# Kernel optimization log

Measured on AMD Instinct MI355X. Metric: run time of the kernel, lower is better.

Reference implementation:

```python
import jax, jax.numpy as jnp
import numpy as np

EMBED_DIM = 1024
HEAD_NUM = 16
HEAD_DIM = EMBED_DIM // HEAD_NUM
T, B, S = 2048, 4, 2048


def setup_inputs() -> dict:
    key = jax.random.key(0)
    ks = jax.random.split(key, 11)
    s = 0.02
    return {
        "query": jax.random.normal(ks[0], (T, B, EMBED_DIM), jnp.float32),
        "key": jax.random.normal(ks[1], (S, B, EMBED_DIM), jnp.float32),
        "value": jax.random.normal(ks[2], (S, B, EMBED_DIM), jnp.float32),
        "q_proj_weight": jax.random.normal(ks[3], (EMBED_DIM, EMBED_DIM), jnp.float32) * s,
        "k_proj_weight": jax.random.normal(ks[4], (EMBED_DIM, EMBED_DIM), jnp.float32) * s,
        "v_proj_weight": jax.random.normal(ks[5], (EMBED_DIM, EMBED_DIM), jnp.float32) * s,
        "in_proj_bias": jax.random.normal(ks[6], (3 * EMBED_DIM,), jnp.float32) * s,
        "bias_k": jax.random.normal(ks[7], (1, 1, EMBED_DIM), jnp.float32) * s,
        "bias_v": jax.random.normal(ks[8], (1, 1, EMBED_DIM), jnp.float32) * s,
        "out_proj_weight": jax.random.normal(ks[9], (EMBED_DIM, EMBED_DIM), jnp.float32) * s,
        "out_proj_bias": jax.random.normal(ks[10], (EMBED_DIM,), jnp.float32) * s,
    }


def reference(query, key, value, q_proj_weight, k_proj_weight, v_proj_weight,
              in_proj_bias, bias_k, bias_v, out_proj_weight, out_proj_bias):
    t, b, e = query.shape
    h, hd = HEAD_NUM, HEAD_DIM
    scaling = float(hd) ** -0.5
    # input projections (F.linear: x @ W.T + b)
    q = (query @ q_proj_weight.T + in_proj_bias[:e]) * scaling          # [T,B,E]
    k = key @ k_proj_weight.T + in_proj_bias[e:2 * e]                   # [S,B,E]
    v = value @ v_proj_weight.T + in_proj_bias[2 * e:]                  # [S,B,E]
    # append bias_k / bias_v token along the sequence dim
    k = jnp.concatenate([k, jnp.broadcast_to(bias_k, (1, b, e))], axis=0)  # [S+1,B,E]
    v = jnp.concatenate([v, jnp.broadcast_to(bias_v, (1, b, e))], axis=0)  # [S+1,B,E]
    # split heads: [L, B, E] -> [B*H, L, hd]
    q = q.reshape(t, b * h, hd).transpose(1, 0, 2)
    k = k.reshape(-1, b * h, hd).transpose(1, 0, 2)
    v = v.reshape(-1, b * h, hd).transpose(1, 0, 2)
    # full O(T*S) attention, as in the original bmm->softmax->bmm
    weights = jax.nn.softmax(jnp.einsum('nqd,nkd->nqk', q, k), axis=-1)  # [B*H,T,S+1]
    out = jnp.einsum('nqk,nkd->nqd', weights, v)                         # [B*H,T,hd]
    out = out.transpose(1, 0, 2).reshape(t, b, e)
    out = out @ out_proj_weight.T + out_proj_bias
    avg_weights = weights.sum(axis=1) / h                                # [B*H,S+1]
    return out, avg_weights
```

## Files before the change

kernel.cpp:

```cpp
#include <hip/hip_runtime.h>

#define T_DIM 2048
#define B_DIM 4
#define S_DIM 2048
#define E_DIM 1024
#define H_NUM 16
#define HD    64
#define NH    64
#define SP1   2049
#define SPAD  2112
#define NCHUNK 33
#define NTOKE ((size_t)T_DIM * B_DIM * E_DIM)

typedef short bf16x8 __attribute__((ext_vector_type(8)));
typedef short bf16x4 __attribute__((ext_vector_type(4)));
typedef float f32x4  __attribute__((ext_vector_type(4)));
typedef float f32x16 __attribute__((ext_vector_type(16)));
typedef unsigned int u32;

#define QSCALE 0.18033688011112042f

#if __has_builtin(__builtin_amdgcn_exp2f)
__device__ __forceinline__ float exp2_fast(float x) { return __builtin_amdgcn_exp2f(x); }
#else
__device__ __forceinline__ float exp2_fast(float x) { return __expf(x * 0.6931471805599453f); }
#endif

__device__ __forceinline__ unsigned short f2bf(float x) {
    union { float f; unsigned int u; } v; v.f = x;
    unsigned int r = v.u + 0x7FFFu + ((v.u >> 16) & 1u);
    return (unsigned short)(r >> 16);
}

__device__ __forceinline__ u32 cvtpk_bf16(float lo, float hi) {
    u32 r;
    asm("v_cvt_pk_bf16_f32 %0, %1, %2" : "=v"(r) : "v"(lo), "v"(hi));
    return r;
}
__device__ __forceinline__ void plswap(u32& a, u32& b) {
    asm("v_permlane32_swap_b32 %0, %1" : "+v"(a), "+v"(b));
}
__device__ __forceinline__ float max3f(float a, float b, float c) {
    float d;
    asm("v_max3_f32 %0, %1, %2, %3" : "=v"(d) : "v"(a), "v"(b), "v"(c));
    return d;
}

__device__ __forceinline__ void load_lds16(const void* g, void* l) {
    __builtin_amdgcn_global_load_lds(
        (const __attribute__((address_space(1))) unsigned int*)g,
        (__attribute__((address_space(3))) unsigned int*)l, 16, 0, 0);
}

__global__ __launch_bounds__(256)
void cvt_all(const float* __restrict__ q, const float* __restrict__ k,
             const float* __restrict__ v, const float* __restrict__ w0,
             const float* __restrict__ w1, const float* __restrict__ w2,
             const float* __restrict__ w3, short* __restrict__ indst,
             short* __restrict__ wdst, short* __restrict__ k_h,
             short* __restrict__ v_h, const float* __restrict__ bias_k,
             const float* __restrict__ bias_v)
{
    const int y = blockIdx.y;
    if (y < 3) {
        const float* src = (y == 0) ? q : (y == 1) ? k : v;
        short* d = indst + (size_t)y * NTOKE;
        const size_t i = (size_t)blockIdx.x * 256 + threadIdx.x;
        const float4* s = reinterpret_cast<const float4*>(src) + i * 2;
        float4 a = s[0], b = s[1];
        uint4 o;
        o.x = cvtpk_bf16(a.x, a.y); o.y = cvtpk_bf16(a.z, a.w);
        o.z = cvtpk_bf16(b.x, b.y); o.w = cvtpk_bf16(b.z, b.w);
        *(reinterpret_cast<uint4*>(d) + i) = o;
    } else {
        const size_t gi = (size_t)blockIdx.x * 256 + threadIdx.x;
        const size_t per = (size_t)E_DIM * E_DIM / 8;
        if (gi < 4 * per) {
            const int wsel = (int)(gi / per);
            const size_t i = gi % per;
            const float* src = (wsel == 0) ? w0 : (wsel == 1) ? w1 : (wsel == 2) ? w2 : w3;
            short* d = wdst + (size_t)wsel * E_DIM * E_DIM;
            const float4* s = reinterpret_cast<const float4*>(src) + i * 2;
            float4 a = s[0], b = s[1];
            uint4 o;
            o.x = cvtpk_bf16(a.x, a.y); o.y = cvtpk_bf16(a.z, a.w);
            o.z = cvtpk_bf16(b.x, b.y); o.w = cvtpk_bf16(b.z, b.w);
            *(reinterpret_cast<uint4*>(d) + i) = o;
        } else {
            const size_t fi = gi - 4 * per;
            if (fi < (size_t)(SPAD - S_DIM) * NH * HD) {
                const int d   = (int)(fi & 63);
                const int row = (int)((fi >> 6) & 63);
                const int n   = (int)(fi >> 12);
                short bk = 0, bv = 0;
                if (row == 0) {
                    bk = (short)f2bf(bias_k[(n & 15) * HD + d]);
                    bv = (short)f2bf(bias_v[(n & 15) * HD + d]);
                }
                const size_t idx = ((size_t)n * SPAD + S_DIM + row) * HD + d;
                k_h[idx] = bk;
                v_h[idx] = bv;
            }
        }
    }
}

__global__ __launch_bounds__(256, 4)
void gemm_qkv(const short* __restrict__ Abase, const short* __restrict__ Wall,
              const float* __restrict__ biasAll, short* __restrict__ outp)
{
    __shared__ short smem[16384];
    short* Asb = smem;
    short* Bsb = smem + 8192;

    const int id = blockIdx.x;
    const int xcd = id & 7;
    const int j = id >> 3;
    const int z = j >> 6;
    const int jj = j & 63;
    const int bm = xcd * 8 + (jj & 7);
    const int bn = jj >> 3;

    const short* Az = Abase + (size_t)z * NTOKE;
    const short* W  = Wall + (size_t)z * E_DIM * E_DIM;
    const float* bias = biasAll + z * E_DIM;

    const int tid = threadIdx.x;
    const int l = tid & 63, w = tid >> 6;
    const int wr = w >> 1, wc = w & 1;
    const int lr = l & 15, lg = l >> 4;
    const int srow = tid >> 2, scol = (tid & 3) * 8;

    auto stage = [&](int b, int k0) {
#pragma unroll
        for (int r = 0; r < 2; ++r) {
            const int row = r * 64 + srow;
            load_lds16(Az + (size_t)(bm * 128 + row) * E_DIM + k0 + scol,
                       Asb + b * 4096 + row * 32 + scol);
            load_lds16(W + (size_t)(bn * 128 + row) * E_DIM + k0 + scol,
                       Bsb + b * 4096 + row * 32 + scol);
        }
    };

    stage(0, 0);
    stage(1, 32);

    f32x4 acc[4][4] = {};
    int buf = 0;

    for (int k0 = 0; k0 < E_DIM; k0 += 32) {
        if (k0 + 32 < E_DIM)
            asm volatile("s_waitcnt vmcnt(4)" ::: "memory");
        else
            asm volatile("s_waitcnt vmcnt(0)" ::: "memory");
        asm volatile("s_barrier" ::: "memory");
        __builtin_amdgcn_sched_barrier(0);

        __builtin_amdgcn_s_setprio(1);
        bf16x8 af[4], bf[4];
#pragma unroll
        for (int mi = 0; mi < 4; ++mi)
            af[mi] = *reinterpret_cast<const bf16x8*>(
                Asb + buf * 4096 + (wr * 64 + mi * 16 + lr) * 32 + lg * 8);
#pragma unroll
        for (int ni = 0; ni < 4; ++ni)
            bf[ni] = *reinterpret_cast<const bf16x8*>(
                Bsb + buf * 4096 + (wc * 64 + ni * 16 + lr) * 32 + lg * 8);
#pragma unroll
        for (int mi = 0; mi < 4; ++mi)
#pragma unroll
            for (int ni = 0; ni < 4; ++ni)
                acc[mi][ni] = __builtin_amdgcn_mfma_f32_16x16x32_bf16(
                    af[mi], bf[ni], acc[mi][ni], 0, 0, 0);
        __builtin_amdgcn_s_setprio(0);

        asm volatile("s_barrier" ::: "memory");
        if (k0 + 64 < E_DIM) stage(buf, k0 + 64);
        buf ^= 1;
    }

#pragma unroll
    for (int mi = 0; mi < 4; ++mi)
#pragma unroll
        for (int ni = 0; ni < 4; ++ni) {
            const int colg = bn * 128 + wc * 64 + ni * 16 + lr;
            const float bv = bias[colg];
            const int cl = wc * 64 + ni * 16 + lr;
#pragma unroll
            for (int r = 0; r < 4; ++r) {
                float v = acc[mi][ni][r] + bv;
                if (z == 0) v *= QSCALE;
                const int rowl = wr * 64 + mi * 16 + lg * 4 + r;
                smem[rowl * 128 + cl] = (short)f2bf(v);
            }
        }
    __syncthreads();

    short* ob = outp;
    if (z == 1) ob += (size_t)NH * T_DIM * HD;
    else if (z == 2) ob += (size_t)NH * T_DIM * HD + (size_t)NH * SPAD * HD;
    const int sd = (z == 0) ? T_DIM : SPAD;
#pragma unroll
    for (int p = 0; p < 8; ++p) {
        const int Ls = p * 2048 + tid * 8;
        const int rowl = Ls >> 7;
        const int col  = Ls & 127;
        const int m = bm * 128 + rowl;
        const int seq = m >> 2, b = m & 3;
        const int colg = bn * 128 + col;
        const int head = colg >> 6, d = colg & 63;
        *reinterpret_cast<uint4*>(ob + ((size_t)(b * 16 + head) * sd + seq) * HD + d) =
            *reinterpret_cast<const uint4*>(smem + Ls);
    }
}

__global__ __launch_bounds__(256, 2)
void gemm_out(const short* __restrict__ o_h, const short* __restrict__ wob,
              const float* __restrict__ out_b, float* __restrict__ out)
{
    __shared__ short As[2][128][64];
    __shared__ short Bs[2][128][64];

    const int id = blockIdx.x;
    const int xcd = id & 7;
    const int j = id >> 3;
    const int bm = xcd * 8 + (j & 7);
    const int bn = j >> 3;

    const int tid = threadIdx.x;
    const int l = tid & 63, w = tid >> 6;
    const int wr = w >> 1, wc = w & 1;
    const int lr = l & 15, lg = l >> 4;
    const int srow = tid >> 3, scol = (tid & 7) * 8;

    auto stage = [&](int b, int k0) {
#pragma unroll
        for (int r = 0; r < 4; ++r) {
            const int row = r * 32 + srow;
            const int m = bm * 128 + row;
            const short* ga = o_h +
                ((size_t)((m & 3) * 16 + (k0 >> 6)) * T_DIM + (m >> 2)) * HD + scol;
            load_lds16(ga, &As[b][row][scol]);
            load_lds16(wob + (size_t)(bn * 128 + row) * E_DIM + k0 + scol, &Bs[b][row][scol]);
        }
    };

    stage(0, 0);
    __syncthreads();

    f32x4 acc[4][4] = {};
    int buf = 0;

    for (int k0 = 0; k0 < E_DIM; k0 += 64) {
        if (k0 + 64 < E_DIM) stage(buf ^ 1, k0 + 64);

        __builtin_amdgcn_s_setprio(1);
#pragma unroll
        for (int c = 0; c < 2; ++c) {
            bf16x8 af[4], bf[4];
#pragma unroll
            for (int mi = 0; mi < 4; ++mi)
                af[mi] = *reinterpret_cast<const bf16x8*>(&As[buf][wr * 64 + mi * 16 + lr][c * 32 + lg * 8]);
#pragma unroll
            for (int ni = 0; ni < 4; ++ni)
                bf[ni] = *reinterpret_cast<const bf16x8*>(&Bs[buf][wc * 64 + ni * 16 + lr][c * 32 + lg * 8]);
#pragma unroll
            for (int mi = 0; mi < 4; ++mi)
#pragma unroll
                for (int ni = 0; ni < 4; ++ni)
                    acc[mi][ni] = __builtin_amdgcn_mfma_f32_16x16x32_bf16(
                        af[mi], bf[ni], acc[mi][ni], 0, 0, 0);
        }
        __builtin_amdgcn_s_setprio(0);
        __syncthreads();
        buf ^= 1;
    }

#pragma unroll
    for (int mi = 0; mi < 4; ++mi)
#pragma unroll
        for (int ni = 0; ni < 4; ++ni) {
            const int colg = bn * 128 + wc * 64 + ni * 16 + lr;
            const float bv = out_b[colg];
#pragma unroll
            for (int r = 0; r < 4; ++r) {
                const int m = bm * 128 + wr * 64 + mi * 16 + lg * 4 + r;
                out[(size_t)m * E_DIM + colg] = acc[mi][ni][r] + bv;
            }
        }
}

__global__ __launch_bounds__(512, 4)
void attn_mfma(const short* __restrict__ q_h, const short* __restrict__ k_h,
               const short* __restrict__ v_h, short* __restrict__ o_h,
               float* __restrict__ m_arr, float* __restrict__ l_arr)
{
    __shared__ short KsD[2][64 * 64];
    __shared__ short VtD[2][64 * 64];

    const int id = blockIdx.x;
    const int xcd = id & 7, slot = id >> 3;
    const int n = xcd * 8 + (slot >> 3);
    const int q0 = (slot & 7) * 256;

    const int tid = threadIdx.x, l = tid & 63, w = tid >> 6;
    const int ql = l & 31;
    const int hi = l >> 5;
    const int qrow = q0 + w * 32 + ql;

    const int krow = tid >> 3, kcg = tid & 7;
    const int kswz = (kcg * 16) ^ ((krow & 7) << 4);
    const int sp = tid & 31, dq = tid >> 5;

    const short* kbase = k_h + (size_t)n * SPAD * HD;
    const short* vbase = v_h + (size_t)n * SPAD * HD;

    bf16x8 aq0, aq1, aq2, aq3;
    {
        const short* qp = q_h + ((size_t)n * T_DIM + qrow) * HD + hi * 8;
        aq0 = *(const bf16x8*)(qp);
        aq1 = *(const bf16x8*)(qp + 16);
        aq2 = *(const bf16x8*)(qp + 32);
        aq3 = *(const bf16x8*)(qp + 48);
    }

    bf16x8 pk  = *(const bf16x8*)(kbase + (size_t)krow * HD + kcg * 8);
    bf16x4 pva = *(const bf16x4*)(vbase + (size_t)(2 * sp) * HD + dq * 4);
    bf16x4 pvb = *(const bf16x4*)(vbase + (size_t)(2 * sp + 1) * HD + dq * 4);
    {
        char* KsB = (char*)KsD[0];
        char* VtB = (char*)VtD[0];
        *(bf16x8*)(KsB + krow * 128 + kswz) = pk;
#pragma unroll
        for (int j = 0; j < 4; ++j) {
            u32 pkd = (u32)(unsigned short)pva[j] | ((u32)(unsigned short)pvb[j] << 16);
            const int d = dq * 4 + j;
            *(u32*)(VtB + d * 128 + ((4 * sp) ^ ((d & 7) << 4))) = pkd;
        }
    }
    __syncthreads();

    float m_run = 0.0f;
    float l_run = 0.0f;
    f32x16 accA, accB;
#pragma unroll
    for (int r = 0; r < 16; ++r) { accA[r] = 0.f; accB[r] = 0.f; }

    for (int kc = 0; kc < NCHUNK; ++kc) {
        const char* KsB = (const char*)KsD[kc & 1];
        const char* VtB = (const char*)VtD[kc & 1];
        const bool more = (kc + 1 < NCHUNK);

        if (more) {
            const int s0n = (kc + 1) * 64;
            pk  = *(const bf16x8*)(kbase + (size_t)(s0n + krow) * HD + kcg * 8);
            pva = *(const bf16x4*)(vbase + (size_t)(s0n + 2 * sp) * HD + dq * 4);
            pvb = *(const bf16x4*)(vbase + (size_t)(s0n + 2 * sp + 1) * HD + dq * 4);
        }

        f32x16 sc0, sc1;
        const float nm = -m_run;
#pragma unroll
        for (int r = 0; r < 16; ++r) { sc0[r] = nm; sc1[r] = nm; }
        __builtin_amdgcn_s_setprio(1);
#pragma unroll
        for (int sl = 0; sl < 4; ++sl) {
            const int cb = ((sl * 32) + hi * 16) ^ ((ql & 7) << 4);
            bf16x8 kf0 = *(const bf16x8*)(KsB + ql * 128 + cb);
            bf16x8 kf1 = *(const bf16x8*)(KsB + (32 + ql) * 128 + cb);
            bf16x8 qf = (sl == 0) ? aq0 : (sl == 1) ? aq1 : (sl == 2) ? aq2 : aq3;
            sc0 = __builtin_amdgcn_mfma_f32_32x32x16_bf16(kf0, qf, sc0, 0, 0, 0);
            sc1 = __builtin_amdgcn_mfma_f32_32x32x16_bf16(kf1, qf, sc1, 0, 0, 0);
        }
        __builtin_amdgcn_s_setprio(0);

        const int s0 = kc * 64;
        if (s0 + 64 > SP1) {
#pragma unroll
            for (int r = 0; r < 16; ++r) {
                const int key = (r & 3) + 8 * (r >> 2) + 4 * hi;
                if (s0 + key >= SP1)      sc0[r] = -1e30f;
                if (s0 + 32 + key >= SP1) sc1[r] = -1e30f;
            }
        }

        float a0 = max3f(sc0[0],  sc0[1],  sc0[2]);
        float a1 = max3f(sc0[3],  sc0[4],  sc0[5]);
        float a2 = max3f(sc0[6],  sc0[7],  sc0[8]);
        float a3 = max3f(sc0[9],  sc0[10], sc0[11]);
        float a4 = max3f(sc0[12], sc0[13], sc0[14]);
        float a5 = max3f(sc0[15], sc1[0],  sc1[1]);
        float a6 = max3f(sc1[2],  sc1[3],  sc1[4]);
        float a7 = max3f(sc1[5],  sc1[6],  sc1[7]);
        float a8 = max3f(sc1[8],  sc1[9],  sc1[10]);
        float a9 = max3f(sc1[11], sc1[12], sc1[13]);
        float aA = fmaxf(sc1[14], sc1[15]);
        float b0 = max3f(a0, a1, a2);
        float b1 = max3f(a3, a4, a5);
        float b2 = max3f(a6, a7, a8);
        float b3 = fmaxf(a9, aA);
        float mxl = fmaxf(max3f(b0, b1, b2), b3);
        const float mx = fmaxf(mxl, __shfl_xor(mxl, 32));
        if (!__all(mx <= 8.0f)) {
            const float sh = fmaxf(mx, 0.0f);
            const float fac = exp2_fast(-sh);
            l_run *= fac;
#pragma unroll
            for (int r = 0; r < 16; ++r) {
                accA[r] *= fac; accB[r] *= fac;
                sc0[r] -= sh;   sc1[r] -= sh;
            }
            m_run += sh;
        }
        float p0[16], p1[16];
#pragma unroll
        for (int r = 0; r < 16; ++r) p0[r] = exp2_fast(sc0[r]);
#pragma unroll
        for (int r = 0; r < 16; ++r) p1[r] = exp2_fast(sc1[r]);
        float sv[16];
#pragma unroll
        for (int r = 0; r < 16; ++r) sv[r] = p0[r] + p1[r];
#pragma unroll
        for (int s = 8; s > 0; s >>= 1)
#pragma unroll
            for (int r = 0; r < s; ++r) sv[r] += sv[r + s];
        l_run += sv[0] + __shfl_xor(sv[0], 32);

        union PF { u32 u[4]; bf16x8 v; };
        PF pf0, pf1, pf2, pf3;
        {
            u32 a0_ = cvtpk_bf16(p0[0], p0[1]),   b0_ = cvtpk_bf16(p0[4], p0[5]);   plswap(a0_, b0_);
            u32 a1_ = cvtpk_bf16(p0[2], p0[3]),   b1_ = cvtpk_bf16(p0[6], p0[7]);   plswap(a1_, b1_);
            u32 a2_ = cvtpk_bf16(p0[8], p0[9]),   b2_ = cvtpk_bf16(p0[12], p0[13]); plswap(a2_, b2_);
            u32 a3_ = cvtpk_bf16(p0[10], p0[11]), b3_ = cvtpk_bf16(p0[14], p0[15]); plswap(a3_, b3_);
            pf0.u[0] = a0_; pf0.u[1] = a1_; pf0.u[2] = b0_; pf0.u[3] = b1_;
            pf1.u[0] = a2_; pf1.u[1] = a3_; pf1.u[2] = b2_; pf1.u[3] = b3_;
            u32 c0_ = cvtpk_bf16(p1[0], p1[1]),   d0_ = cvtpk_bf16(p1[4], p1[5]);   plswap(c0_, d0_);
            u32 c1_ = cvtpk_bf16(p1[2], p1[3]),   d1_ = cvtpk_bf16(p1[6], p1[7]);   plswap(c1_, d1_);
            u32 c2_ = cvtpk_bf16(p1[8], p1[9]),   d2_ = cvtpk_bf16(p1[12], p1[13]); plswap(c2_, d2_);
            u32 c3_ = cvtpk_bf16(p1[10], p1[11]), d3_ = cvtpk_bf16(p1[14], p1[15]); plswap(c3_, d3_);
            pf2.u[0] = c0_; pf2.u[1] = c1_; pf2.u[2] = d0_; pf2.u[3] = d1_;
            pf3.u[0] = c2_; pf3.u[1] = c3_; pf3.u[2] = d2_; pf3.u[3] = d3_;
        }

        __builtin_amdgcn_s_setprio(1);
#pragma unroll
        for (int ksl = 0; ksl < 4; ++ksl) {
            const int cb = ((ksl * 32) + hi * 16) ^ ((ql & 7) << 4);
            bf16x8 vf0 = *(const bf16x8*)(VtB + ql * 128 + cb);
            bf16x8 vf1 = *(const bf16x8*)(VtB + (32 + ql) * 128 + cb);
            const bf16x8 pv = (ksl == 0) ? pf0.v : (ksl == 1) ? pf1.v : (ksl == 2) ? pf2.v : pf3.v;
            accA = __builtin_amdgcn_mfma_f32_32x32x16_bf16(vf0, pv, accA, 0, 0, 0);
            accB = __builtin_amdgcn_mfma_f32_32x32x16_bf16(vf1, pv, accB, 0, 0, 0);
        }
        __builtin_amdgcn_s_setprio(0);

        if (more) {
            char* KsN = (char*)KsD[(kc & 1) ^ 1];
            char* VtN = (char*)VtD[(kc & 1) ^ 1];
            *(bf16x8*)(KsN + krow * 128 + kswz) = pk;
#pragma unroll
            for (int j = 0; j < 4; ++j) {
                u32 pkd = (u32)(unsigned short)pva[j] | ((u32)(unsigned short)pvb[j] << 16);
                const int d = dq * 4 + j;
                *(u32*)(VtN + d * 128 + ((4 * sp) ^ ((d & 7) << 4))) = pkd;
            }
            __syncthreads();
        }
    }

    const float il = 1.0f / l_run;
    short* orow = o_h + ((size_t)n * T_DIM + qrow) * HD;
#pragma unroll
    for (int rq = 0; rq < 4; ++rq) {
        uint2 st;
        st.x = cvtpk_bf16(accA[rq * 4 + 0] * il, accA[rq * 4 + 1] * il);
        st.y = cvtpk_bf16(accA[rq * 4 + 2] * il, accA[rq * 4 + 3] * il);
        *(uint2*)(orow + rq * 8 + hi * 4) = st;
        uint2 st2;
        st2.x = cvtpk_bf16(accB[rq * 4 + 0] * il, accB[rq * 4 + 1] * il);
        st2.y = cvtpk_bf16(accB[rq * 4 + 2] * il, accB[rq * 4 + 3] * il);
        *(uint2*)(orow + 32 + rq * 8 + hi * 4) = st2;
    }
    if (hi == 0) {
        m_arr[n * T_DIM + qrow] = m_run;
        l_arr[n * T_DIM + qrow] = l_run;
    }
}

__global__ __launch_bounds__(256)
void colsum_mfma(const short* __restrict__ q_h, const short* __restrict__ k_h,
                 const float* __restrict__ m_arr, const float* __restrict__ l_arr,
                 float* __restrict__ avg_out)
{
    __shared__ short Qs[2][64][72];
    __shared__ float msh[2][64];
    __shared__ float lih[2][64];

    const int id = blockIdx.x;
    const int xcd = id & 7, slot = id >> 3;
    const int n = xcd * 8 + slot / 33;
    const int s0 = (slot % 33) * 64;

    const int tid = threadIdx.x, l = tid & 63, w = tid >> 6;
    const int lr = l & 15, lg = l >> 4;
    const int qr = tid >> 3, qcg = tid & 7;

    const short* qbase = q_h + (size_t)n * T_DIM * HD;

    bf16x8 ak[2];
#pragma unroll
    for (int c = 0; c < 2; ++c)
        ak[c] = *reinterpret_cast<const bf16x8*>(
            k_h + ((size_t)n * SPAD + s0 + w * 16 + lr) * HD + c * 32 + lg * 8);

    bf16x8 qa = *(const bf16x8*)(qbase + (size_t)qr * HD + qcg * 8);
    bf16x8 qb = *(const bf16x8*)(qbase + (size_t)(32 + qr) * HD + qcg * 8);
    float mlv = 0.f;
    if (tid < 64) mlv = m_arr[n * T_DIM + tid];
    else if (tid < 128) mlv = l_arr[n * T_DIM + tid - 64];
    *(bf16x8*)&Qs[0][qr][qcg * 8] = qa;
    *(bf16x8*)&Qs[0][32 + qr][qcg * 8] = qb;
    if (tid < 64) msh[0][tid] = mlv;
    else if (tid < 128) lih[0][tid - 64] = 1.0f / mlv;
    __syncthreads();

    float csum[4] = {0.f, 0.f, 0.f, 0.f};

    for (int it = 0; it < T_DIM / 64; ++it) {
        const int buf = it & 1;
        const bool more = (it + 1 < T_DIM / 64);
        if (more) {
            const int qo = (it + 1) * 64;
            qa = *(const bf16x8*)(qbase + (size_t)(qo + qr) * HD + qcg * 8);
            qb = *(const bf16x8*)(qbase + (size_t)(qo + 32 + qr) * HD + qcg * 8);
            if (tid < 64) mlv = m_arr[n * T_DIM + qo + tid];
            else if (tid < 128) mlv = l_arr[n * T_DIM + qo + tid - 64];
        }
        __builtin_amdgcn_s_setprio(1);
#pragma unroll
        for (int qt = 0; qt < 4; ++qt) {
            bf16x8 bq0 = *reinterpret_cast<const bf16x8*>(&Qs[buf][qt * 16 + lr][lg * 8]);
            bf16x8 bq1 = *reinterpret_cast<const bf16x8*>(&Qs[buf][qt * 16 + lr][32 + lg * 8]);
            const float mq = msh[buf][qt * 16 + lr];
            const float lq = lih[buf][qt * 16 + lr];
            f32x4 z;
#pragma unroll
            for (int r = 0; r < 4; ++r) z[r] = -mq;
            z = __builtin_amdgcn_mfma_f32_16x16x32_bf16(ak[0], bq0, z, 0, 0, 0);
            z = __builtin_amdgcn_mfma_f32_16x16x32_bf16(ak[1], bq1, z, 0, 0, 0);
#pragma unroll
            for (int r = 0; r < 4; ++r)
                csum[r] += exp2_fast(z[r]) * lq;
        }
        __builtin_amdgcn_s_setprio(0);
        if (more) {
            *(bf16x8*)&Qs[buf ^ 1][qr][qcg * 8] = qa;
            *(bf16x8*)&Qs[buf ^ 1][32 + qr][qcg * 8] = qb;
            if (tid < 64) msh[buf ^ 1][tid] = mlv;
            else if (tid < 128) lih[buf ^ 1][tid - 64] = 1.0f / mlv;
            __syncthreads();
        }
    }

#pragma unroll
    for (int r = 0; r < 4; ++r) {
        float v = csum[r];
        v += __shfl_xor(v, 1, 16);
        v += __shfl_xor(v, 2, 16);
        v += __shfl_xor(v, 4, 16);
        v += __shfl_xor(v, 8, 16);
        if (lr == 0) {
            const int key = s0 + w * 16 + lg * 4 + r;
            if (key < SP1) avg_out[(size_t)n * SP1 + key] = v * 0.0625f;
        }
    }
}

extern "C" void kernel_launch(void* const* d_in, const int* in_sizes, int n_in,
                              void* d_out, int out_size, void* d_ws, size_t ws_size,
                              hipStream_t stream)
{
    const float* query   = (const float*)d_in[0];
    const float* key     = (const float*)d_in[1];
    const float* value   = (const float*)d_in[2];
    const float* wq      = (const float*)d_in[3];
    const float* wk      = (const float*)d_in[4];
    const float* wv      = (const float*)d_in[5];
    const float* in_bias = (const float*)d_in[6];
    const float* bias_k  = (const float*)d_in[7];
    const float* bias_v  = (const float*)d_in[8];
    const float* wo      = (const float*)d_in[9];
    const float* out_b   = (const float*)d_in[10];
    float* out = (float*)d_out;

    short* wqb    = (short*)d_ws;
    short* wob    = wqb + (size_t)3 * E_DIM * E_DIM;
    short* qkv_bf = wqb + (size_t)4 * E_DIM * E_DIM;
    short* q_h = qkv_bf + 3 * NTOKE;
    short* k_h = q_h + (size_t)NH * T_DIM * HD;
    short* v_h = k_h + (size_t)NH * SPAD * HD;
    short* o_h = v_h + (size_t)NH * SPAD * HD;
    float* m_arr = (float*)(o_h + (size_t)NH * T_DIM * HD);
    float* l_arr = m_arr + (size_t)NH * T_DIM;

    const dim3 blk(256);
    hipLaunchKernelGGL(cvt_all, dim3(4096, 4), blk, 0, stream,
                       query, key, value, wq, wk, wv, wo, qkv_bf, wqb,
                       k_h, v_h, bias_k, bias_v);

    hipLaunchKernelGGL(gemm_qkv, dim3(1536), blk, 0, stream,
                       qkv_bf, wqb, in_bias, q_h);
    hipLaunchKernelGGL(attn_mfma, dim3(512), dim3(512), 0, stream,
                       q_h, k_h, v_h, o_h, m_arr, l_arr);
    hipLaunchKernelGGL(colsum_mfma, dim3(2112), blk, 0, stream,
                       q_h, k_h, m_arr, l_arr, out + (size_t)T_DIM * B_DIM * E_DIM);
    hipLaunchKernelGGL(gemm_out, dim3(512), blk, 0, stream,
                       o_h, wob, out_b, out);
}
```

Before: 275.1 us.

## Software-pipeline attention loop: overlap next QK MFMA with previous softmax and PV

```diff
diff --git a/kernel.cpp b/kernel.cpp
--- a/kernel.cpp
+++ b/kernel.cpp
@@ -290,7 +290,7 @@
         }
 }
 
-__global__ __launch_bounds__(512, 4)
+__global__ __launch_bounds__(512, 2)
 void attn_mfma(const short* __restrict__ q_h, const short* __restrict__ k_h,
                const short* __restrict__ v_h, short* __restrict__ o_h,
                float* __restrict__ m_arr, float* __restrict__ l_arr)
@@ -332,9 +332,9 @@
         char* VtB = (char*)VtD[0];
         *(bf16x8*)(KsB + krow * 128 + kswz) = pk;
 #pragma unroll
-        for (int j = 0; j < 4; ++j) {
-            u32 pkd = (u32)(unsigned short)pva[j] | ((u32)(unsigned short)pvb[j] << 16);
-            const int d = dq * 4 + j;
+        for (int jj = 0; jj < 4; ++jj) {
+            u32 pkd = (u32)(unsigned short)pva[jj] | ((u32)(unsigned short)pvb[jj] << 16);
+            const int d = dq * 4 + jj;
             *(u32*)(VtB + d * 128 + ((4 * sp) ^ ((d & 7) << 4))) = pkd;
         }
     }
@@ -343,12 +343,11 @@
     float m_run = 0.0f;
     float l_run = 0.0f;
     f32x16 accA, accB;
-#pragma unroll
-    for (int r = 0; r < 16; ++r) { accA[r] = 0.f; accB[r] = 0.f; }
+    f32x16 sP0, sP1;
+#pragma unroll
+    for (int r = 0; r < 16; ++r) { accA[r] = 0.f; accB[r] = 0.f; sP0[r] = 0.f; sP1[r] = 0.f; }
 
     for (int kc = 0; kc < NCHUNK; ++kc) {
-        const char* KsB = (const char*)KsD[kc & 1];
-        const char* VtB = (const char*)VtD[kc & 1];
         const bool more = (kc + 1 < NCHUNK);
 
         if (more) {
@@ -358,10 +357,11 @@
             pvb = *(const bf16x4*)(vbase + (size_t)(s0n + 2 * sp + 1) * HD + dq * 4);
         }
 
-        f32x16 sc0, sc1;
+        const char* KsB = (const char*)KsD[kc & 1];
+        f32x16 sN0, sN1;
         const float nm = -m_run;
 #pragma unroll
-        for (int r = 0; r < 16; ++r) { sc0[r] = nm; sc1[r] = nm; }
+        for (int r = 0; r < 16; ++r) { sN0[r] = nm; sN1[r] = nm; }
         __builtin_amdgcn_s_setprio(1);
 #pragma unroll
         for (int sl = 0; sl < 4; ++sl) {
@@ -369,32 +369,124 @@
             bf16x8 kf0 = *(const bf16x8*)(KsB + ql * 128 + cb);
             bf16x8 kf1 = *(const bf16x8*)(KsB + (32 + ql) * 128 + cb);
             bf16x8 qf = (sl == 0) ? aq0 : (sl == 1) ? aq1 : (sl == 2) ? aq2 : aq3;
-            sc0 = __builtin_amdgcn_mfma_f32_32x32x16_bf16(kf0, qf, sc0, 0, 0, 0);
-            sc1 = __builtin_amdgcn_mfma_f32_32x32x16_bf16(kf1, qf, sc1, 0, 0, 0);
+            sN0 = __builtin_amdgcn_mfma_f32_32x32x16_bf16(kf0, qf, sN0, 0, 0, 0);
+            sN1 = __builtin_amdgcn_mfma_f32_32x32x16_bf16(kf1, qf, sN1, 0, 0, 0);
         }
         __builtin_amdgcn_s_setprio(0);
 
-        const int s0 = kc * 64;
-        if (s0 + 64 > SP1) {
+        const int s0c = kc * 64;
+        if (s0c + 64 > SP1) {
 #pragma unroll
             for (int r = 0; r < 16; ++r) {
                 const int key = (r & 3) + 8 * (r >> 2) + 4 * hi;
-                if (s0 + key >= SP1)      sc0[r] = -1e30f;
-                if (s0 + 32 + key >= SP1) sc1[r] = -1e30f;
-            }
-        }
-
-        float a0 = max3f(sc0[0],  sc0[1],  sc0[2]);
-        float a1 = max3f(sc0[3],  sc0[4],  sc0[5]);
-        float a2 = max3f(sc0[6],  sc0[7],  sc0[8]);
-        float a3 = max3f(sc0[9],  sc0[10], sc0[11]);
-        float a4 = max3f(sc0[12], sc0[13], sc0[14]);
-        float a5 = max3f(sc0[15], sc1[0],  sc1[1]);
-        float a6 = max3f(sc1[2],  sc1[3],  sc1[4]);
-        float a7 = max3f(sc1[5],  sc1[6],  sc1[7]);
-        float a8 = max3f(sc1[8],  sc1[9],  sc1[10]);
-        float a9 = max3f(sc1[11], sc1[12], sc1[13]);
-        float aA = fmaxf(sc1[14], sc1[15]);
+                if (s0c + key >= SP1)      sN0[r] = -1e30f;
+                if (s0c + 32 + key >= SP1) sN1[r] = -1e30f;
+            }
+        }
+
+        if (kc > 0) {
+            float a0 = max3f(sP0[0],  sP0[1],  sP0[2]);
+            float a1 = max3f(sP0[3],  sP0[4],  sP0[5]);
+            float a2 = max3f(sP0[6],  sP0[7],  sP0[8]);
+            float a3 = max3f(sP0[9],  sP0[10], sP0[11]);
+            float a4 = max3f(sP0[12], sP0[13], sP0[14]);
+            float a5 = max3f(sP0[15], sP1[0],  sP1[1]);
+            float a6 = max3f(sP1[2],  sP1[3],  sP1[4]);
+            float a7 = max3f(sP1[5],  sP1[6],  sP1[7]);
+            float a8 = max3f(sP1[8],  sP1[9],  sP1[10]);
+            float a9 = max3f(sP1[11], sP1[12], sP1[13]);
+            float aA = fmaxf(sP1[14], sP1[15]);
+            float b0 = max3f(a0, a1, a2);
+            float b1 = max3f(a3, a4, a5);
+            float b2 = max3f(a6, a7, a8);
+            float b3 = fmaxf(a9, aA);
+            float mxl = fmaxf(max3f(b0, b1, b2), b3);
+            const float mx = fmaxf(mxl, __shfl_xor(mxl, 32));
+            if (!__all(mx <= 8.0f)) {
+                const float sh = fmaxf(mx, 0.0f);
+                const float fac = exp2_fast(-sh);
+                l_run *= fac;
+#pragma unroll
+                for (int r = 0; r < 16; ++r) {
+                    accA[r] *= fac; accB[r] *= fac;
+                    sP0[r] -= sh;   sP1[r] -= sh;
+                    sN0[r] -= sh;   sN1[r] -= sh;
+                }
+                m_run += sh;
+            }
+#pragma unroll
+            for (int r = 0; r < 16; ++r) sP0[r] = exp2_fast(sP0[r]);
+#pragma unroll
+            for (int r = 0; r < 16; ++r) sP1[r] = exp2_fast(sP1[r]);
+            float sv[16];
+#pragma unroll
+            for (int r = 0; r < 16; ++r) sv[r] = sP0[r] + sP1[r];
+#pragma unroll
+            for (int s = 8; s > 0; s >>= 1)
+#pragma unroll
+                for (int r = 0; r < s; ++r) sv[r] += sv[r + s];
+            l_run += sv[0] + __shfl_xor(sv[0], 32);
+
+            union PF { u32 u[4]; bf16x8 v; };
+            PF pf0, pf1, pf2, pf3;
+            {
+                u32 a0_ = cvtpk_bf16(sP0[0], sP0[1]),   b0_ = cvtpk_bf16(sP0[4], sP0[5]);   plswap(a0_, b0_);
+                u32 a1_ = cvtpk_bf16(sP0[2], sP0[3]),   b1_ = cvtpk_bf16(sP0[6], sP0[7]);   plswap(a1_, b1_);
+                u32 a2_ = cvtpk_bf16(sP0[8], sP0[9]),   b2_ = cvtpk_bf16(sP0[12], sP0[13]); plswap(a2_, b2_);
+                u32 a3_ = cvtpk_bf16(sP0[10], sP0[11]), b3_ = cvtpk_bf16(sP0[14], sP0[15]); plswap(a3_, b3_);
+                pf0.u[0] = a0_; pf0.u[1] = a1_; pf0.u[2] = b0_; pf0.u[3] = b1_;
+                pf1.u[0] = a2_; pf1.u[1] = a3_; pf1.u[2] = b2_; pf1.u[3] = b3_;
+                u32 c0_ = cvtpk_bf16(sP1[0], sP1[1]),   d0_ = cvtpk_bf16(sP1[4], sP1[5]);   plswap(c0_, d0_);
+                u32 c1_ = cvtpk_bf16(sP1[2], sP1[3]),   d1_ = cvtpk_bf16(sP1[6], sP1[7]);   plswap(c1_, d1_);
+                u32 c2_ = cvtpk_bf16(sP1[8], sP1[9]),   d2_ = cvtpk_bf16(sP1[12], sP1[13]); plswap(c2_, d2_);
+                u32 c3_ = cvtpk_bf16(sP1[10], sP1[11]), d3_ = cvtpk_bf16(sP1[14], sP1[15]); plswap(c3_, d3_);
+                pf2.u[0] = c0_; pf2.u[1] = c1_; pf2.u[2] = d0_; pf2.u[3] = d1_;
+                pf3.u[0] = c2_; pf3.u[1] = c3_; pf3.u[2] = d2_; pf3.u[3] = d3_;
+            }
+
+            const char* VtP = (const char*)VtD[(kc - 1) & 1];
+            __builtin_amdgcn_s_setprio(1);
+#pragma unroll
+            for (int ksl = 0; ksl < 4; ++ksl) {
+                const int cb = ((ksl * 32) + hi * 16) ^ ((ql & 7) << 4);
+                bf16x8 vf0 = *(const bf16x8*)(VtP + ql * 128 + cb);
+                bf16x8 vf1 = *(const bf16x8*)(VtP + (32 + ql) * 128 + cb);
+                const bf16x8 pv = (ksl == 0) ? pf0.v : (ksl == 1) ? pf1.v : (ksl == 2) ? pf2.v : pf3.v;
+                accA = __builtin_amdgcn_mfma_f32_32x32x16_bf16(vf0, pv, accA, 0, 0, 0);
+                accB = __builtin_amdgcn_mfma_f32_32x32x16_bf16(vf1, pv, accB, 0, 0, 0);
+            }
+            __builtin_amdgcn_s_setprio(0);
+        }
+
+        if (more) {
+            __syncthreads();
+            char* KsN = (char*)KsD[(kc + 1) & 1];
+            char* VtN = (char*)VtD[(kc + 1) & 1];
+            *(bf16x8*)(KsN + krow * 128 + kswz) = pk;
+#pragma unroll
+            for (int jj = 0; jj < 4; ++jj) {
+                u32 pkd = (u32)(unsigned short)pva[jj] | ((u32)(unsigned short)pvb[jj] << 16);
+                const int d = dq * 4 + jj;
+                *(u32*)(VtN + d * 128 + ((4 * sp) ^ ((d & 7) << 4))) = pkd;
+            }
+            __syncthreads();
+        }
+
+        sP0 = sN0; sP1 = sN1;
+    }
+
+    {
+        float a0 = max3f(sP0[0],  sP0[1],  sP0[2]);
+        float a1 = max3f(sP0[3],  sP0[4],  sP0[5]);
+        float a2 = max3f(sP0[6],  sP0[7],  sP0[8]);
+        float a3 = max3f(sP0[9],  sP0[10], sP0[11]);
+        float a4 = max3f(sP0[12], sP0[13], sP0[14]);
+        float a5 = max3f(sP0[15], sP1[0],  sP1[1]);
+        float a6 = max3f(sP1[2],  sP1[3],  sP1[4]);
+        float a7 = max3f(sP1[5],  sP1[6],  sP1[7]);
+        float a8 = max3f(sP1[8],  sP1[9],  sP1[10]);
+        float a9 = max3f(sP1[11], sP1[12], sP1[13]);
+        float aA = fmaxf(sP1[14], sP1[15]);
         float b0 = max3f(a0, a1, a2);
         float b1 = max3f(a3, a4, a5);
         float b2 = max3f(a6, a7, a8);
@@ -408,18 +500,17 @@
 #pragma unroll
             for (int r = 0; r < 16; ++r) {
                 accA[r] *= fac; accB[r] *= fac;
-                sc0[r] -= sh;   sc1[r] -= sh;
+                sP0[r] -= sh;   sP1[r] -= sh;
             }
             m_run += sh;
         }
-        float p0[16], p1[16];
-#pragma unroll
-        for (int r = 0; r < 16; ++r) p0[r] = exp2_fast(sc0[r]);
-#pragma unroll
-        for (int r = 0; r < 16; ++r) p1[r] = exp2_fast(sc1[r]);
+#pragma unroll
+        for (int r = 0; r < 16; ++r) sP0[r] = exp2_fast(sP0[r]);
+#pragma unroll
+        for (int r = 0; r < 16; ++r) sP1[r] = exp2_fast(sP1[r]);
         float sv[16];
 #pragma unroll
-        for (int r = 0; r < 16; ++r) sv[r] = p0[r] + p1[r];
+        for (int r = 0; r < 16; ++r) sv[r] = sP0[r] + sP1[r];
 #pragma unroll
         for (int s = 8; s > 0; s >>= 1)
 #pragma unroll
@@ -429,44 +520,32 @@
         union PF { u32 u[4]; bf16x8 v; };
         PF pf0, pf1, pf2, pf3;
         {
-            u32 a0_ = cvtpk_bf16(p0[0], p0[1]),   b0_ = cvtpk_bf16(p0[4], p0[5]);   plswap(a0_, b0_);
-            u32 a1_ = cvtpk_bf16(p0[2], p0[3]),   b1_ = cvtpk_bf16(p0[6], p0[7]);   plswap(a1_, b1_);
-            u32 a2_ = cvtpk_bf16(p0[8], p0[9]),   b2_ = cvtpk_bf16(p0[12], p0[13]); plswap(a2_, b2_);
-            u32 a3_ = cvtpk_bf16(p0[10], p0[11]), b3_ = cvtpk_bf16(p0[14], p0[15]); plswap(a3_, b3_);
+            u32 a0_ = cvtpk_bf16(sP0[0], sP0[1]),   b0_ = cvtpk_bf16(sP0[4], sP0[5]);   plswap(a0_, b0_);
+            u32 a1_ = cvtpk_bf16(sP0[2], sP0[3]),   b1_ = cvtpk_bf16(sP0[6], sP0[7]);   plswap(a1_, b1_);
+            u32 a2_ = cvtpk_bf16(sP0[8], sP0[9]),   b2_ = cvtpk_bf16(sP0[12], sP0[13]); plswap(a2_, b2_);
+            u32 a3_ = cvtpk_bf16(sP0[10], sP0[11]), b3_ = cvtpk_bf16(sP0[14], sP0[15]); plswap(a3_, b3_);
             pf0.u[0] = a0_; pf0.u[1] = a1_; pf0.u[2] = b0_; pf0.u[3] = b1_;
             pf1.u[0] = a2_; pf1.u[1] = a3_; pf1.u[2] = b2_; pf1.u[3] = b3_;
-            u32 c0_ = cvtpk_bf16(p1[0], p1[1]),   d0_ = cvtpk_bf16(p1[4], p1[5]);   plswap(c0_, d0_);
-            u32 c1_ = cvtpk_bf16(p1[2], p1[3]),   d1_ = cvtpk_bf16(p1[6], p1[7]);   plswap(c1_, d1_);
-            u32 c2_ = cvtpk_bf16(p1[8], p1[9]),   d2_ = cvtpk_bf16(p1[12], p1[13]); plswap(c2_, d2_);
-            u32 c3_ = cvtpk_bf16(p1[10], p1[11]), d3_ = cvtpk_bf16(p1[14], p1[15]); plswap(c3_, d3_);
+            u32 c0_ = cvtpk_bf16(sP1[0], sP1[1]),   d0_ = cvtpk_bf16(sP1[4], sP1[5]);   plswap(c0_, d0_);
+            u32 c1_ = cvtpk_bf16(sP1[2], sP1[3]),   d1_ = cvtpk_bf16(sP1[6], sP1[7]);   plswap(c1_, d1_);
+            u32 c2_ = cvtpk_bf16(sP1[8], sP1[9]),   d2_ = cvtpk_bf16(sP1[12], sP1[13]); plswap(c2_, d2_);
+            u32 c3_ = cvtpk_bf16(sP1[10], sP1[11]), d3_ = cvtpk_bf16(sP1[14], sP1[15]); plswap(c3_, d3_);
             pf2.u[0] = c0_; pf2.u[1] = c1_; pf2.u[2] = d0_; pf2.u[3] = d1_;
             pf3.u[0] = c2_; pf3.u[1] = c3_; pf3.u[2] = d2_; pf3.u[3] = d3_;
         }
 
+        const char* VtP = (const char*)VtD[(NCHUNK - 1) & 1];
         __builtin_amdgcn_s_setprio(1);
 #pragma unroll
         for (int ksl = 0; ksl < 4; ++ksl) {
             const int cb = ((ksl * 32) + hi * 16) ^ ((ql & 7) << 4);
-            bf16x8 vf0 = *(const bf16x8*)(VtB + ql * 128 + cb);
-            bf16x8 vf1 = *(const bf16x8*)(VtB + (32 + ql) * 128 + cb);
+            bf16x8 vf0 = *(const bf16x8*)(VtP + ql * 128 + cb);
+            bf16x8 vf1 = *(const bf16x8*)(VtP + (32 + ql) * 128 + cb);
             const bf16x8 pv = (ksl == 0) ? pf0.v : (ksl == 1) ? pf1.v : (ksl == 2) ? pf2.v : pf3.v;
             accA = __builtin_amdgcn_mfma_f32_32x32x16_bf16(vf0, pv, accA, 0, 0, 0);
             accB = __builtin_amdgcn_mfma_f32_32x32x16_bf16(vf1, pv, accB, 0, 0, 0);
         }
         __builtin_amdgcn_s_setprio(0);
-
-        if (more) {
-            char* KsN = (char*)KsD[(kc & 1) ^ 1];
-            char* VtN = (char*)VtD[(kc & 1) ^ 1];
-            *(bf16x8*)(KsN + krow * 128 + kswz) = pk;
-#pragma unroll
-            for (int j = 0; j < 4; ++j) {
-                u32 pkd = (u32)(unsigned short)pva[j] | ((u32)(unsigned short)pvb[j] << 16);
-                const int d = dq * 4 + j;
-                *(u32*)(VtN + d * 128 + ((4 * sp) ^ ((d & 7) << 4))) = pkd;
-            }
-            __syncthreads();
-        }
     }
 
     const float il = 1.0f / l_run;
```

New measurement: 287.7 us. 4.6% more time.
